# Optimization experiments

Measured on AMD Instinct MI355X. Metric: run time of the kernel, lower is better.

Reference implementation:

```python
import jax, jax.numpy as jnp
import numpy as np

B, T, I, E, K, J = 4, 4096, 1024, 16, 512, 1024

def setup_inputs() -> dict:
    key = jax.random.key(0)
    k1, k2, k3 = jax.random.split(key, 3)
    X = jax.random.normal(k1, (B, T, I), dtype=jnp.float32)
    ind = jax.random.randint(k2, (B, E, K), 0, T, dtype=jnp.int64)
    W = jax.random.normal(k3, (E, I, J), dtype=jnp.float32)
    return {"X": X, "ind": ind, "W": W}

def reference(X, ind, W):
    b, t, i = X.shape
    # offset each batch's indices into the flattened [B*T, I] token table
    offset = jnp.arange(b, dtype=ind.dtype)[:, None, None] * t  # [B,1,1]
    X_flat = X.reshape(b * t, i)
    X_gathered = X_flat[ind + offset]  # [B,E,K,I] irregular gather
    Y = jnp.einsum('beki,eij->bekj', X_gathered, W)  # grouped GEMM per expert
    return Y
```

## Files before the change

### kernel.cpp

```cpp
#include <hip/hip_runtime.h>

#define DI __device__ __forceinline__

constexpr int Bc = 4, Tc = 4096, Ic = 1024, Ec = 16, Kc = 512, Jc = 1024;

typedef __attribute__((ext_vector_type(8))) short short8;
typedef __attribute__((ext_vector_type(4))) float floatx4;

DI unsigned pack2_bf16(float a, float b) {
  union { float f; unsigned u; } ua, ub;
  ua.f = a; ub.f = b;
  const unsigned x = ua.u + 0x8000u;
  const unsigned y = ub.u + 0x8000u;
#if __has_builtin(__builtin_amdgcn_perm)
  return __builtin_amdgcn_perm(y, x, 0x07060302u);
#else
  return (x >> 16) | (y & 0xFFFF0000u);
#endif
}

DI void async_load16(const void* g, void* lds) {
  __builtin_amdgcn_global_load_lds((const __attribute__((address_space(1))) void*)g,
                                   (__attribute__((address_space(3))) void*)lds,
                                   16, 0, 0);
}

__global__ __launch_bounds__(256) void gather_cast(const float* __restrict__ X,
                                                   const int* __restrict__ ind,
                                                   unsigned short* __restrict__ Xg) {
  const int row = blockIdx.x;
  const int t = threadIdx.x;
  const int b = row >> 13;
  const int r = ind[row];
  const float4 v = *(const float4*)(X + ((size_t)(b * Tc + r)) * Ic + t * 4);
  uint2 u;
  u.x = pack2_bf16(v.x, v.y);
  u.y = pack2_bf16(v.z, v.w);
  *(uint2*)(Xg + (size_t)row * Ic + t * 4) = u;
}

__global__ __launch_bounds__(256) void transpose_w(const float* __restrict__ W,
                                                   unsigned short* __restrict__ Wt) {
  __shared__ float tile[32][129];
  const int bid = blockIdx.x;
  const int kk = bid & 31;
  const int jt = (bid >> 5) & 7;
  const int e  = bid >> 8;
  const int t  = threadIdx.x;

  const float* Wp = W + ((size_t)(e * Ic + kk * 32)) * Jc + jt * 128;
#pragma unroll
  for (int p = 0; p < 4; ++p) {
    const int il = p * 8 + (t >> 5);
    const int c4 = (t & 31) * 4;
    const float4 v = *(const float4*)(Wp + (size_t)il * Jc + c4);
    tile[il][c4 + 0] = v.x; tile[il][c4 + 1] = v.y;
    tile[il][c4 + 2] = v.z; tile[il][c4 + 3] = v.w;
  }
  __syncthreads();

  unsigned short* out = Wt + ((size_t)((e * 8 + jt) * 32 + kk)) * 4096;
#pragma unroll
  for (int h = 0; h < 2; ++h) {
    const int n   = h * 64 + (t >> 2);
    const int il0 = (t & 3) * 8;
    unsigned u[4];
#pragma unroll
    for (int q = 0; q < 4; ++q)
      u[q] = pack2_bf16(tile[il0 + 2 * q][n], tile[il0 + 2 * q + 1][n]);
    *(uint4*)(out + (size_t)(h * 256 + t) * 8) = *(uint4*)u;
  }
}

__global__ __launch_bounds__(256) void moe_gemm(const unsigned short* __restrict__ Xg,
                                                const unsigned short* __restrict__ Wt,
                                                float* __restrict__ Y) {
  __shared__ unsigned short As[128 * 32];
  __shared__ unsigned short Bs[128 * 32];

  const int bid = blockIdx.x;
  const int jt = bid & 7;
  const int kt = (bid >> 3) & 3;
  const int e  = (bid >> 5) & 15;
  const int b  = bid >> 9;

  const int t = threadIdx.x;
  const int w = t >> 6;
  const int l = t & 63;
  const int nl  = l >> 2;
  const int csw = (l & 3) ^ (nl & 3);

  const int R0 = (b * Ec + e) * Kc + kt * 128;
  const unsigned short* asrc[2];
  const unsigned short* bsrc[2];
  unsigned short* adst[2];
  unsigned short* bdst[2];
#pragma unroll
  for (int p = 0; p < 2; ++p) {
    const int rg = w * 2 + p;
    asrc[p] = Xg + (size_t)(R0 + rg * 16 + nl) * Ic + csw * 8;
    bsrc[p] = Wt + ((size_t)((e * 8 + jt) * 32)) * 4096 + rg * 512 + nl * 32 + csw * 8;
    adst[p] = &As[rg * 512];
    bdst[p] = &Bs[rg * 512];
  }

  floatx4 acc[4][4];
#pragma unroll
  for (int tm = 0; tm < 4; ++tm)
#pragma unroll
    for (int tn = 0; tn < 4; ++tn) acc[tm][tn] = (floatx4){0.f, 0.f, 0.f, 0.f};

  const int wm = (w & 1) * 64;
  const int wn = (w >> 1) * 64;
  const int lrow = l & 15;
  const int quad = l >> 4;
  const int swz  = lrow & 3;

  for (int kk = 0; kk < Ic / 32; ++kk) {
    __syncthreads();
#pragma unroll
    for (int p = 0; p < 2; ++p) {
      async_load16(asrc[p] + kk * 32, adst[p]);
      async_load16(bsrc[p] + (size_t)kk * 4096, bdst[p]);
    }
    __syncthreads();

    short8 af[4], bf[4];
#pragma unroll
    for (int tm = 0; tm < 4; ++tm)
      af[tm] = *(const short8*)&As[(wm + tm * 16 + lrow) * 32 + (quad ^ swz) * 8];
#pragma unroll
    for (int tn = 0; tn < 4; ++tn)
      bf[tn] = *(const short8*)&Bs[(wn + tn * 16 + lrow) * 32 + (quad ^ swz) * 8];
#pragma unroll
    for (int tm = 0; tm < 4; ++tm)
#pragma unroll
      for (int tn = 0; tn < 4; ++tn)
        acc[tm][tn] = __builtin_amdgcn_mfma_f32_16x16x32_bf16(af[tm], bf[tn], acc[tm][tn], 0, 0, 0);
  }

  float* Yp = Y + ((size_t)(b * Ec + e) * Kc + (size_t)kt * 128) * Jc + jt * 128;
#pragma unroll
  for (int tm = 0; tm < 4; ++tm) {
#pragma unroll
    for (int tn = 0; tn < 4; ++tn) {
#pragma unroll
      for (int r = 0; r < 4; ++r) {
        const int row = wm + tm * 16 + quad * 4 + r;
        const int col = wn + tn * 16 + lrow;
        Yp[(size_t)row * Jc + col] = acc[tm][tn][r];
      }
    }
  }
}

extern "C" void kernel_launch(void* const* d_in, const int* in_sizes, int n_in,
                              void* d_out, int out_size, void* d_ws, size_t ws_size,
                              hipStream_t stream) {
  const float* X = (const float*)d_in[0];
  const int* ind = (const int*)d_in[1];
  const float* W = (const float*)d_in[2];
  float* Y = (float*)d_out;

  unsigned short* Xg = (unsigned short*)d_ws;
  unsigned short* Wt = (unsigned short*)d_ws + (size_t)Bc * Ec * Kc * Ic;

  hipLaunchKernelGGL(gather_cast, dim3(Bc * Ec * Kc), dim3(256), 0, stream, X, ind, Xg);
  hipLaunchKernelGGL(transpose_w, dim3(Ec * 8 * 32), dim3(256), 0, stream, W, Wt);
  hipLaunchKernelGGL(moe_gemm, dim3(Bc * Ec * 4 * 8), dim3(256), 0, stream, Xg, Wt, Y);
}
```

Before: 355.7 us.

## Fuse gather and weight transpose into one prep kernel with tiled X layout

Merges the gather-cast and weight-transpose kernels into a single launch that alternates block roles. The gathered X is written through LDS into a tiled layout of contiguous 128x32 bf16 chunks, matching the weight layout, so GEMM A loads become contiguous. The GEMM now stages two K-slices per barrier pair, halving synchronisations, and reorders block indices so jt is the slowest dimension, which changes cache reuse. This costs more LDS per GEMM block and adds an LDS round-trip in the gather.

```diff
diff --git a/kernel.cpp b/kernel.cpp
--- a/kernel.cpp
+++ b/kernel.cpp
@@ -25,64 +25,81 @@
                                    16, 0, 0);
 }
 
-__global__ __launch_bounds__(256) void gather_cast(const float* __restrict__ X,
-                                                   const int* __restrict__ ind,
-                                                   unsigned short* __restrict__ Xg) {
-  const int row = blockIdx.x;
+__global__ __launch_bounds__(256) void prep(const float* __restrict__ X,
+                                            const int* __restrict__ ind,
+                                            const float* __restrict__ W,
+                                            unsigned short* __restrict__ Xg,
+                                            unsigned short* __restrict__ Wt) {
+  __shared__ __align__(16) char smem[32 * 260 * 2];
+  const int bid = blockIdx.x >> 1;
   const int t = threadIdx.x;
-  const int b = row >> 13;
-  const int r = ind[row];
-  const float4 v = *(const float4*)(X + ((size_t)(b * Tc + r)) * Ic + t * 4);
-  uint2 u;
-  u.x = pack2_bf16(v.x, v.y);
-  u.y = pack2_bf16(v.z, v.w);
-  *(uint2*)(Xg + (size_t)row * Ic + t * 4) = u;
-}
 
-__global__ __launch_bounds__(256) void transpose_w(const float* __restrict__ W,
-                                                   unsigned short* __restrict__ Wt) {
-  __shared__ float tile[32][129];
-  const int bid = blockIdx.x;
-  const int kk = bid & 31;
-  const int jt = (bid >> 5) & 7;
-  const int e  = bid >> 8;
-  const int t  = threadIdx.x;
-
-  const float* Wp = W + ((size_t)(e * Ic + kk * 32)) * Jc + jt * 128;
+  if ((blockIdx.x & 1) == 0) {
+    unsigned short* Ls = (unsigned short*)smem;
+    const int g = t >> 5, kk = t & 31;
+    const int R = bid * 8 + g;
+    const int b = R >> 13;
+    const int xr = ind[R];
+    const float* src = X + ((size_t)(b * Tc + xr)) * Ic + kk * 32;
+    unsigned u[16];
 #pragma unroll
-  for (int p = 0; p < 4; ++p) {
-    const int il = p * 8 + (t >> 5);
-    const int c4 = (t & 31) * 4;
-    const float4 v = *(const float4*)(Wp + (size_t)il * Jc + c4);
-    tile[il][c4 + 0] = v.x; tile[il][c4 + 1] = v.y;
-    tile[il][c4 + 2] = v.z; tile[il][c4 + 3] = v.w;
-  }
-  __syncthreads();
-
-  unsigned short* out = Wt + ((size_t)((e * 8 + jt) * 32 + kk)) * 4096;
+    for (int q = 0; q < 8; ++q) {
+      const float4 v = *(const float4*)(src + q * 4);
+      u[2 * q]     = pack2_bf16(v.x, v.y);
+      u[2 * q + 1] = pack2_bf16(v.z, v.w);
+    }
+    unsigned short* lp = &Ls[kk * 260 + g * 32];
 #pragma unroll
-  for (int h = 0; h < 2; ++h) {
-    const int n   = h * 64 + (t >> 2);
-    const int il0 = (t & 3) * 8;
-    unsigned u[4];
+    for (int q = 0; q < 4; ++q) *(uint4*)(lp + q * 8) = *(uint4*)&u[4 * q];
+    __syncthreads();
+    const int kk2 = t >> 3, rw = t & 7;
+    const int tt = bid >> 4;
+    const int rl0 = (bid & 15) * 8;
+    unsigned short* dst = Xg + ((size_t)(tt * 32 + kk2) * 128 + rl0 + rw) * 32;
+    const unsigned short* lr = &Ls[kk2 * 260 + rw * 32];
 #pragma unroll
-    for (int q = 0; q < 4; ++q)
-      u[q] = pack2_bf16(tile[il0 + 2 * q][n], tile[il0 + 2 * q + 1][n]);
-    *(uint4*)(out + (size_t)(h * 256 + t) * 8) = *(uint4*)u;
+    for (int q = 0; q < 4; ++q) *(uint4*)(dst + q * 8) = *(const uint4*)(lr + q * 8);
+  } else {
+    float (*tile)[129] = (float(*)[129])smem;
+    const int kk = bid & 31;
+    const int jt = (bid >> 5) & 7;
+    const int e  = bid >> 8;
+    const float* Wp = W + ((size_t)(e * Ic + kk * 32)) * Jc + jt * 128;
+#pragma unroll
+    for (int p = 0; p < 4; ++p) {
+      const int il = p * 8 + (t >> 5);
+      const int c4 = (t & 31) * 4;
+      const float4 v = *(const float4*)(Wp + (size_t)il * Jc + c4);
+      tile[il][c4 + 0] = v.x; tile[il][c4 + 1] = v.y;
+      tile[il][c4 + 2] = v.z; tile[il][c4 + 3] = v.w;
+    }
+    __syncthreads();
+    unsigned short* out = Wt + ((size_t)((e * 8 + jt) * 32 + kk)) * 4096;
+#pragma unroll
+    for (int h = 0; h < 2; ++h) {
+      const int n   = h * 64 + (t >> 2);
+      const int il0 = (t & 3) * 8;
+      unsigned u[4];
+#pragma unroll
+      for (int q = 0; q < 4; ++q)
+        u[q] = pack2_bf16(tile[il0 + 2 * q][n], tile[il0 + 2 * q + 1][n]);
+      *(uint4*)(out + (size_t)(h * 256 + t) * 8) = *(uint4*)u;
+    }
   }
 }
 
 __global__ __launch_bounds__(256) void moe_gemm(const unsigned short* __restrict__ Xg,
                                                 const unsigned short* __restrict__ Wt,
                                                 float* __restrict__ Y) {
-  __shared__ unsigned short As[128 * 32];
-  __shared__ unsigned short Bs[128 * 32];
+  __shared__ unsigned short As[2 * 128 * 32];
+  __shared__ unsigned short Bs[2 * 128 * 32];
 
   const int bid = blockIdx.x;
-  const int jt = bid & 7;
-  const int kt = (bid >> 3) & 3;
-  const int e  = (bid >> 5) & 15;
-  const int b  = bid >> 9;
+  const int jt = bid >> 8;
+  const int rr = bid & 255;
+  const int b  = rr >> 6;
+  const int e  = (rr >> 2) & 15;
+  const int kt = rr & 3;
 
   const int t = threadIdx.x;
   const int w = t >> 6;
@@ -90,16 +107,16 @@
   const int nl  = l >> 2;
   const int csw = (l & 3) ^ (nl & 3);
 
-  const int R0 = (b * Ec + e) * Kc + kt * 128;
-  const unsigned short* asrc[2];
-  const unsigned short* bsrc[2];
-  unsigned short* adst[2];
-  unsigned short* bdst[2];
+  const int atile = (b * Ec + e) * 4 + kt;
+  const unsigned short* abase = Xg + (size_t)atile * 32 * 4096;
+  const unsigned short* bbase = Wt + (size_t)((e * 8 + jt) * 32) * 4096;
+
+  int loff[2];
+  unsigned short *adst[2], *bdst[2];
 #pragma unroll
   for (int p = 0; p < 2; ++p) {
     const int rg = w * 2 + p;
-    asrc[p] = Xg + (size_t)(R0 + rg * 16 + nl) * Ic + csw * 8;
-    bsrc[p] = Wt + ((size_t)((e * 8 + jt) * 32)) * 4096 + rg * 512 + nl * 32 + csw * 8;
+    loff[p] = (rg * 16 + nl) * 32 + csw * 8;
     adst[p] = &As[rg * 512];
     bdst[p] = &Bs[rg * 512];
   }
@@ -116,27 +133,34 @@
   const int quad = l >> 4;
   const int swz  = lrow & 3;
 
-  for (int kk = 0; kk < Ic / 32; ++kk) {
+  for (int kk2 = 0; kk2 < 16; ++kk2) {
     __syncthreads();
 #pragma unroll
-    for (int p = 0; p < 2; ++p) {
-      async_load16(asrc[p] + kk * 32, adst[p]);
-      async_load16(bsrc[p] + (size_t)kk * 4096, bdst[p]);
+    for (int s = 0; s < 2; ++s) {
+      const size_t cb = (size_t)(kk2 * 2 + s) * 4096;
+#pragma unroll
+      for (int p = 0; p < 2; ++p) {
+        async_load16(abase + cb + loff[p], adst[p] + s * 4096);
+        async_load16(bbase + cb + loff[p], bdst[p] + s * 4096);
+      }
     }
     __syncthreads();
 
-    short8 af[4], bf[4];
 #pragma unroll
-    for (int tm = 0; tm < 4; ++tm)
-      af[tm] = *(const short8*)&As[(wm + tm * 16 + lrow) * 32 + (quad ^ swz) * 8];
+    for (int s = 0; s < 2; ++s) {
+      short8 af[4], bf[4];
 #pragma unroll
-    for (int tn = 0; tn < 4; ++tn)
-      bf[tn] = *(const short8*)&Bs[(wn + tn * 16 + lrow) * 32 + (quad ^ swz) * 8];
-#pragma unroll
-    for (int tm = 0; tm < 4; ++tm)
+      for (int tm = 0; tm < 4; ++tm)
+        af[tm] = *(const short8*)&As[s * 4096 + (wm + tm * 16 + lrow) * 32 + (quad ^ swz) * 8];
 #pragma unroll
       for (int tn = 0; tn < 4; ++tn)
-        acc[tm][tn] = __builtin_amdgcn_mfma_f32_16x16x32_bf16(af[tm], bf[tn], acc[tm][tn], 0, 0, 0);
+        bf[tn] = *(const short8*)&Bs[s * 4096 + (wn + tn * 16 + lrow) * 32 + (quad ^ swz) * 8];
+#pragma unroll
+      for (int tm = 0; tm < 4; ++tm)
+#pragma unroll
+        for (int tn = 0; tn < 4; ++tn)
+          acc[tm][tn] = __builtin_amdgcn_mfma_f32_16x16x32_bf16(af[tm], bf[tn], acc[tm][tn], 0, 0, 0);
+    }
   }
 
   float* Yp = Y + ((size_t)(b * Ec + e) * Kc + (size_t)kt * 128) * Jc + jt * 128;
@@ -165,7 +189,6 @@
   unsigned short* Xg = (unsigned short*)d_ws;
   unsigned short* Wt = (unsigned short*)d_ws + (size_t)Bc * Ec * Kc * Ic;
 
-  hipLaunchKernelGGL(gather_cast, dim3(Bc * Ec * Kc), dim3(256), 0, stream, X, ind, Xg);
-  hipLaunchKernelGGL(transpose_w, dim3(Ec * 8 * 32), dim3(256), 0, stream, W, Wt);
+  hipLaunchKernelGGL(prep, dim3(8192), dim3(256), 0, stream, X, ind, W, Xg, Wt);
   hipLaunchKernelGGL(moe_gemm, dim3(Bc * Ec * 4 * 8), dim3(256), 0, stream, Xg, Wt, Y);
 }
```

Measured after the change: 350.1 us. No clear change (-1.6%).
